# Kernel optimization log

Measured on AMD Instinct MI355X. Metric: run time of the kernel, lower is better.

## Reference

```python
import jax, jax.numpy as jnp
import numpy as np

NUM_CLASSES = 2
CONF_THRESH = 0.05
NMS_THRESH = 0.3
NMS_TOP_K = 5000
TOP_K = 750
VAR0, VAR1 = 0.1, 0.2
NEG = -1e9  # sentinel for suppressed / below-threshold scores

NUM = 16
PRIORS = 131072


def setup_inputs() -> dict:
    key = jax.random.key(0)
    k1, k2, k3 = jax.random.split(key, 3)
    loc_data = jax.random.normal(k1, (NUM, PRIORS, 4), dtype=jnp.float32)
    conf_data = jax.random.uniform(k2, (NUM * PRIORS, NUM_CLASSES), dtype=jnp.float32)
    prior_data = jax.random.uniform(k3, (PRIORS, 4), dtype=jnp.float32)
    return {"loc_data": loc_data, "conf_data": conf_data, "prior_data": prior_data}


def decode(loc, priors):
    # loc, priors: [N, 4] (cx, cy, w, h priors); SSD box decode -> (x1, y1, x2, y2)
    xy = priors[:, :2] + loc[:, :2] * VAR0 * priors[:, 2:]
    wh = priors[:, 2:] * jnp.exp(loc[:, 2:] * VAR1)
    return jnp.concatenate([xy - wh * 0.5, xy + wh * 0.5], axis=-1)


def _area(b):
    return (b[..., 2] - b[..., 0]) * (b[..., 3] - b[..., 1])


def iou_one_to_many(box, boxes):
    # box: [4], boxes: [K, 4]
    lt = jnp.maximum(box[:2], boxes[:, :2])
    rb = jnp.minimum(box[2:], boxes[:, 2:])
    wh = jnp.clip(rb - lt, 0.0)
    inter = wh[:, 0] * wh[:, 1]
    union = _area(box) + _area(boxes) - inter
    return inter / jnp.maximum(union, 1e-12)


def nms_single(boxes, scores):
    # boxes: [P, 4], scores: [P] (one image, one class) -> [TOP_K, 5] (score, x1, y1, x2, y2)
    s = jnp.where(scores > CONF_THRESH, scores, NEG)
    top_s, top_i = jax.lax.top_k(s, NMS_TOP_K)
    top_b = boxes[top_i]  # [K, 4]
    idx_range = jnp.arange(NMS_TOP_K)

    def step(s_work, _):
        idx = jnp.argmax(s_work)
        sc = s_work[idx]
        valid = sc > NEG * 0.5
        box = top_b[idx]
        ious = iou_one_to_many(box, top_b)
        kill = (ious > NMS_THRESH) | (idx_range == idx)
        s_new = jnp.where(kill, NEG, s_work)
        row = jnp.where(valid, jnp.concatenate([sc[None], box]), jnp.zeros((5,), boxes.dtype))
        return s_new, row

    _, rows = jax.lax.scan(step, top_s, None, length=TOP_K)
    return rows  # [TOP_K, 5]


def reference(loc_data, conf_data, prior_data):
    num, P, _ = loc_data.shape
    conf = conf_data.reshape(num, P, NUM_CLASSES).transpose(0, 2, 1)  # [num, C, P]
    batch_priors = jnp.broadcast_to(prior_data, (num, P, 4)).reshape(-1, 4)
    boxes = decode(loc_data.reshape(-1, 4), batch_priors).reshape(num, P, 4)
    # NMS over non-background classes, vmapped over batch and class
    per_image = jax.vmap(nms_single, in_axes=(None, 0))          # over classes
    det = jax.vmap(per_image)(boxes, conf[:, 1:, :])             # [num, C-1, TOP_K, 5]
    bg = jnp.zeros((num, 1, TOP_K, 5), det.dtype)
    return jnp.concatenate([bg, det], axis=1)                     # [num, C, TOP_K, 5]
```

## Files before the change

kernel.cpp:

```cpp
#include <hip/hip_runtime.h>
#include <cmath>

#pragma clang fp contract(off)

typedef unsigned long long ull;
typedef unsigned int uint;

#define NPRIORS 131072
#define NIMG 16
#define KSEL 5000
#define TOPK 750
#define SORTN 8192
#define MW 80
#define NCHUNK 79
#define KSELP (NCHUNK * 64)
#define NBIN 65536

#define MID03 0.30000002682209014892578125

#define WS_PAIRS 0
#define WS_NDIAG 0
#define WS_MCNT 1048576
#define WS_BOXES 1048832
#define WS_SCORES 2328832
#define WS_MASK 2649088
#define WS_HIST (WS_MASK)
#define WS_CNT  (WS_MASK + 4194304)
#define WS_POS  (WS_MASK + 8388608)
#define WS_DIAG (WS_MASK + (size_t)NIMG * KSEL * MW * 8)

__device__ inline ull readlane64(ull t, int l) {
  unsigned lo = (unsigned)__builtin_amdgcn_readlane((int)(unsigned)t, l);
  unsigned hi = (unsigned)__builtin_amdgcn_readlane((int)(unsigned)(t >> 32), l);
  return ((ull)hi << 32) | lo;
}

__device__ inline void softBarrier() {
  asm volatile("s_waitcnt lgkmcnt(0)\n\ts_barrier" ::: "memory");
}

__global__ __launch_bounds__(256) void hist_kernel(const float* __restrict__ conf,
                                                   unsigned int* __restrict__ hist) {
  const int img = blockIdx.y;
  const float4* c4 = (const float4*)conf + (size_t)img * (NPRIORS / 2);
  unsigned int* H = hist + (size_t)img * NBIN;
  for (int q = blockIdx.x * 256 + threadIdx.x; q < NPRIORS / 2; q += 64 * 256) {
    float4 v = c4[q];
    if (v.y > 0.05f) atomicAdd(&H[(__float_as_uint(v.y) >> 12) & 0xFFFFu], 1u);
    if (v.w > 0.05f) atomicAdd(&H[(__float_as_uint(v.w) >> 12) & 0xFFFFu], 1u);
  }
}

__global__ __launch_bounds__(1024) void cutoff_kernel(const unsigned int* __restrict__ hist,
                                                      unsigned int* __restrict__ pos,
                                                      int* __restrict__ meta,
                                                      float4* __restrict__ sboxes,
                                                      float* __restrict__ sscores) {
  const int img = blockIdx.x;
  const int tid = threadIdx.x;
  const int lane = tid & 63;
  const int wv = tid >> 6;
  const unsigned int* H = hist + (size_t)img * NBIN;
  unsigned int* P = pos + (size_t)img * NBIN;
  __shared__ unsigned int csum[1024];
  __shared__ unsigned int suf[1024];
  __shared__ int s_cc;
  __shared__ unsigned int s_cut, s_mc;

  for (int g = 0; g < 64; ++g) {
    unsigned int v = H[g * 1024 + tid];
    for (int m = 1; m < 64; m <<= 1) v += __shfl_xor(v, m);
    if (lane == 0) csum[g * 16 + wv] = v;
  }
  __syncthreads();
  suf[tid] = csum[tid];
  if (tid == 0) s_cc = 0;
  __syncthreads();
  for (int off = 1; off < 1024; off <<= 1) {
    unsigned int v = (tid + off < 1024) ? suf[tid + off] : 0u;
    __syncthreads();
    suf[tid] += v;
    __syncthreads();
  }
  if (suf[tid] >= KSEL && (suf[tid] - csum[tid]) < KSEL) s_cc = tid;
  __syncthreads();
  const int cc = s_cc;
  if (tid == 0) { s_cut = (unsigned int)(cc * 64); s_mc = suf[0]; }
  __syncthreads();
  for (int b = cc * 64 + tid; b < NBIN; b += 1024) {
    int q = b >> 6;
    unsigned int acc = (q + 1 < 1024) ? suf[q + 1] : 0u;
    for (int b2 = b + 1; b2 < (q + 1) * 64; ++b2) acc += H[b2];
    P[b] = acc;
    unsigned int h = H[b];
    if (acc < KSEL && acc + h >= KSEL) { s_cut = (unsigned int)b; s_mc = acc + h; }
  }
  __syncthreads();
  if (tid == 0) {
    meta[img] = (int)min(s_mc, (unsigned int)SORTN);
    meta[16 + img] = (int)s_cut;
  }
  for (int i = tid; i < KSEL; i += 1024) {
    sboxes[(size_t)img * KSEL + i] = make_float4(0.f, 0.f, 0.f, 0.f);
    sscores[(size_t)img * KSEL + i] = -1e9f;
  }
}

__global__ __launch_bounds__(256) void scatter_kernel(const float* __restrict__ conf,
                                                      const unsigned int* __restrict__ pos,
                                                      unsigned int* __restrict__ cnt,
                                                      const int* __restrict__ meta,
                                                      ull* __restrict__ pairs) {
  const int img = blockIdx.y;
  const float4* c4 = (const float4*)conf + (size_t)img * (NPRIORS / 2);
  const unsigned int* P = pos + (size_t)img * NBIN;
  unsigned int* Cn = cnt + (size_t)img * NBIN;
  ull* mypairs = pairs + (size_t)img * SORTN;
  const unsigned int cutval = ((unsigned int)meta[16 + img]) << 12;
  for (int q = blockIdx.x * 256 + threadIdx.x; q < NPRIORS / 2; q += 64 * 256) {
    float4 v = c4[q];
#pragma unroll
    for (int h = 0; h < 2; ++h) {
      float sc = h ? v.w : v.y;
      unsigned int p = 2 * (unsigned int)q + h;
      if (sc > 0.05f) {
        unsigned int u = __float_as_uint(sc);
        if (u >= cutval) {
          unsigned int bin = (u >> 12) & 0xFFFFu;
          unsigned int slot = atomicAdd(&Cn[bin], 1u);
          unsigned int idx = P[bin] + slot;
          if (idx < SORTN)
            mypairs[idx] = ((ull)u << 32) | (ull)(0xFFFFFFFFu - p);
        }
      }
    }
  }
}

__global__ __launch_bounds__(256) void rank_decode_kernel(const ull* __restrict__ pairs,
                                                          const unsigned int* __restrict__ hist,
                                                          const unsigned int* __restrict__ pos,
                                                          const int* __restrict__ meta,
                                                          const float* __restrict__ loc,
                                                          const float* __restrict__ prior,
                                                          float4* __restrict__ sboxes,
                                                          float* __restrict__ sscores) {
#pragma clang fp contract(off)
  const int img = blockIdx.y;
  const int s = blockIdx.x * 256 + threadIdx.x;
  const int mc = meta[img];
  if (s >= mc) return;
  const ull* mypairs = pairs + (size_t)img * SORTN;
  const ull key = mypairs[s];
  const unsigned int u = (unsigned int)(key >> 32);
  const unsigned int bin = (u >> 12) & 0xFFFFu;
  const unsigned int base = pos[(size_t)img * NBIN + bin];
  const unsigned int cb = hist[(size_t)img * NBIN + bin];
  const int end = min((int)(base + cb), mc);
  int rank = 0;
  for (int j = (int)base; j < end; ++j) rank += (mypairs[j] > key);
  const int fp = (int)base + rank;
  if (fp >= KSEL) return;
  const unsigned int p = 0xFFFFFFFFu - (unsigned int)(key & 0xFFFFFFFFu);
  const float* lp = loc + ((size_t)img * NPRIORS + p) * 4;
  const float* pp = prior + (size_t)p * 4;
  float l0 = lp[0], l1 = lp[1], l2 = lp[2], l3 = lp[3];
  float px = pp[0], py = pp[1], pw = pp[2], ph = pp[3];
  float cx = px + (l0 * 0.1f) * pw;
  float cy = py + (l1 * 0.1f) * ph;
  float w = pw * (float)exp((double)(l2 * 0.2f));
  float hh = ph * (float)exp((double)(l3 * 0.2f));
  float4 box;
  box.x = cx - w * 0.5f;
  box.y = cy - hh * 0.5f;
  box.z = cx + w * 0.5f;
  box.w = cy + hh * 0.5f;
  sboxes[(size_t)img * KSEL + fp] = box;
  sscores[(size_t)img * KSEL + fp] = __uint_as_float(u);
}

__global__ __launch_bounds__(256) void mask_build_kernel(const float4* __restrict__ sboxes,
                                                         ull* __restrict__ mask,
                                                         ull* __restrict__ diag,
                                                         ull* __restrict__ ndiag) {
#pragma clang fp contract(off)
  const int jt = blockIdx.x;
  const int rt = blockIdx.y;
  const int img = blockIdx.z;
  if (jt < rt) return;
  const int tid = threadIdx.x;
  const int lane = tid & 63;
  const int wv = __builtin_amdgcn_readfirstlane(tid >> 6);
  const float4* bb = sboxes + (size_t)img * KSEL;

  __shared__ float4 cbox[256];
  __shared__ float carea[256];
  {
    int j = jt * 256 + tid;
    float4 c = (j < KSEL) ? bb[j] : make_float4(0.f, 0.f, 0.f, 0.f);
    cbox[tid] = c;
    carea[tid] = (c.z - c.x) * (c.w - c.y);
  }
  __syncthreads();

  const int R = rt * 256 + wv * 64;
  if (R >= KSEL) return;
  const int i = R + lane;
  float4 pb = (i < KSEL) ? bb[i] : make_float4(0.f, 0.f, 0.f, 0.f);
  const float pa = (pb.z - pb.x) * (pb.w - pb.y);

  auto killbit = [&](int j) -> uint {
    float4 c = cbox[j];
    float caa = carea[j];
    float ltx = fmaxf(pb.x, c.x), lty = fmaxf(pb.y, c.y);
    float rbx = fminf(pb.z, c.z), rby = fminf(pb.w, c.w);
    float ww = fmaxf(rbx - ltx, 0.0f), hh = fmaxf(rby - lty, 0.0f);
    float inter = ww * hh;
    float uni = fmaxf(pa + caa - inter, 1e-12f);
    float f = fmaf(-0.3f, uni, inter);
    float band = uni * 0x1p-20f;
    bool kill = f > band;
    if (__builtin_expect(__ballot(fabsf(f) <= band) != 0ULL, 0)) {
      if (fabsf(f) <= band) kill = (double)inter > MID03 * (double)uni;
    }
    return kill ? 1u : 0u;
  };

  uint wl[4], wh[4];
#pragma unroll
  for (int s = 0; s < 4; ++s) {
    if (jt == rt && s < wv) { wl[s] = 0u; wh[s] = 0u; continue; }
    uint alo = 0, ahi = 0;
#pragma unroll 8
    for (int b = 0; b < 32; ++b) alo |= killbit(s * 64 + b) << b;
#pragma unroll 8
    for (int b = 0; b < 32; ++b) ahi |= killbit(s * 64 + 32 + b) << b;
    wl[s] = alo; wh[s] = ahi;
  }

  if (jt == rt) {
    uint mlo, mhi;
    if (lane < 32) { mlo = 0xFFFFFFFEu << lane; mhi = 0xFFFFFFFFu; }
    else           { mlo = 0u; mhi = 0xFFFFFFFEu << (lane - 32); }
    uint dl, dh;
    if (wv == 0)      { wl[0] &= mlo; wh[0] &= mhi; dl = wl[0]; dh = wh[0]; }
    else if (wv == 1) { wl[1] &= mlo; wh[1] &= mhi; dl = wl[1]; dh = wh[1]; }
    else if (wv == 2) { wl[2] &= mlo; wh[2] &= mhi; dl = wl[2]; dh = wh[2]; }
    else              { wl[3] &= mlo; wh[3] &= mhi; dl = wl[3]; dh = wh[3]; }
    if (i < KSEL) {
      diag[(size_t)img * KSELP + i] = ((ull)dh << 32) | dl;
      if (wv < 3) {
        uint nl, nh;
        if (wv == 0)      { nl = wl[1]; nh = wh[1]; }
        else if (wv == 1) { nl = wl[2]; nh = wh[2]; }
        else              { nl = wl[3]; nh = wh[3]; }
        ndiag[(size_t)img * KSELP + i] = ((ull)nh << 32) | nl;
      }
    }
  }
  if (jt == rt + 1 && wv == 3 && i < KSEL)
    ndiag[(size_t)img * KSELP + i] = ((ull)wh[0] << 32) | wl[0];

  if (i < KSEL) {
    uint* wp = (uint*)(mask + (size_t)img * KSEL * MW + (size_t)i * MW) + jt * 8;
    *(uint4*)wp = make_uint4(wl[0], wh[0], wl[1], wh[1]);
    *((uint4*)wp + 1) = make_uint4(wl[2], wh[2], wl[3], wh[3]);
  }
}

__global__ __launch_bounds__(128) void sweep_kernel(const ull* __restrict__ mask,
                                                    const ull* __restrict__ diag,
                                                    const ull* __restrict__ ndiag,
                                                    const float4* __restrict__ sboxes,
                                                    const float* __restrict__ sscores,
                                                    const int* __restrict__ meta,
                                                    float* __restrict__ out) {
  const int img = blockIdx.x;
  const int tid = threadIdx.x;
  const int lane = tid & 63;
  const bool waveA = (tid < 64);
  const int V = min(meta[img], KSEL);
  const ull* mb = mask + (size_t)img * KSEL * MW;
  const ull* dg = diag + (size_t)img * KSELP;
  const ull* ng = ndiag + (size_t)img * KSELP;
  __shared__ ull mailbox[NCHUNK + 1];
  __shared__ int pickbuf[TOPK];
  __shared__ int s_np[NCHUNK];
  __shared__ int s_start[NCHUNK];
  __shared__ int s_done;
  __shared__ int s_n;
  const int lc = min(lane, 39);

  for (int i = tid; i <= NCHUNK; i += 128) mailbox[i] = 0ULL;
  if (tid == 0) { s_done = 0; s_n = 0; }
  __syncthreads();

  if (V > 0) {
    ull dw = 0, ndw = 0, bridge = 0;
    ull rlo = 0, rhi = 0;
    int nkeep = 0;
    bool adone = false;
    if (waveA) { dw = dg[lane]; ndw = ng[lane]; }

    for (int k = 0; k < NCHUNK; ++k) {
      softBarrier();
      if (s_done) break;
      if (waveA) {
        if (!adone) {
          const int base = k * 64;
          const int nidx = min(base + 64 + lane, KSELP - 1);
          ull dwn = dg[nidx];
          ull ndwn = ng[nidx];
          ull cur = mailbox[k] | bridge;
          bridge = 0ULL;
          const int lim = V - base;
          ull validm = (lim >= 64) ? ~0ULL : ((~0ULL) >> (64 - lim));
          ull avail = (~cur) & validm;
          const int st = nkeep;
          if (lane == 0) s_start[k] = st;
          while (avail != 0ULL && nkeep < TOPK) {
            int r = __builtin_ctzll(avail);
            if (lane == 0) pickbuf[nkeep] = base + r;
            nkeep++;
            ull dr = readlane64(dw, r);
            bridge |= readlane64(ndw, r);
            avail &= ~(dr | (1ULL << r));
          }
          if (lane == 0) s_np[k] = nkeep - st;
          if (nkeep >= TOPK || base + 64 >= V) {
            if (lane == 0) { s_done = 1; s_n = (nkeep < TOPK) ? nkeep : TOPK; }
            adone = true;
          }
          dw = dwn;
          ndw = ndwn;
        }
      } else if (k >= 1) {
        const int np = s_np[k - 1];
        const int st = s_start[k - 1];
        for (int g = 0; g < np; g += 16) {
          ulonglong2 v[16];
#pragma unroll
          for (int q = 0; q < 16; ++q) {
            int t = min(g + q, np - 1);
            int row = pickbuf[st + t];
            v[q] = *(const ulonglong2*)(mb + (size_t)row * MW + 2 * lc);
          }
#pragma unroll
          for (int q = 0; q < 16; ++q) { rlo |= v[q].x; rhi |= v[q].y; }
        }
        const int w = k + 1;
        if (w < NCHUNK) {
          ull t = (w & 1) ? rhi : rlo;
          ull word = readlane64(t, w >> 1);
          if (lane == 0) mailbox[w] = word;
        }
      }
    }
  }

  __syncthreads();
  const int n = s_n;
  float* ob = out + (size_t)img * (2 * TOPK * 5) + TOPK * 5;
  for (int j = tid; j < n; j += 128) {
    int i = pickbuf[j];
    float4 b = sboxes[(size_t)img * KSEL + i];
    float sc = sscores[(size_t)img * KSEL + i];
    float* o = ob + (size_t)j * 5;
    o[0] = sc; o[1] = b.x; o[2] = b.y; o[3] = b.z; o[4] = b.w;
  }
}

extern "C" void kernel_launch(void* const* d_in, const int* in_sizes, int n_in,
                              void* d_out, int out_size, void* d_ws, size_t ws_size,
                              hipStream_t stream) {
  const float* loc = (const float*)d_in[0];
  const float* conf = (const float*)d_in[1];
  const float* prior = (const float*)d_in[2];
  float* out = (float*)d_out;

  char* ws = (char*)d_ws;
  ull* pairs = (ull*)(ws + WS_PAIRS);
  ull* ndiag = (ull*)(ws + WS_NDIAG);
  int* meta = (int*)(ws + WS_MCNT);
  float4* sboxes = (float4*)(ws + WS_BOXES);
  float* sscores = (float*)(ws + WS_SCORES);
  ull* mask = (ull*)(ws + WS_MASK);
  ull* diag = (ull*)(ws + WS_DIAG);
  unsigned int* hist = (unsigned int*)(ws + WS_HIST);
  unsigned int* cnt = (unsigned int*)(ws + WS_CNT);
  unsigned int* pos = (unsigned int*)(ws + WS_POS);

  hipMemsetAsync(d_out, 0, (size_t)out_size * sizeof(float), stream);
  hipMemsetAsync(ws + WS_HIST, 0, 2u * 4194304u, stream);

  {
    dim3 g(64, NIMG);
    hist_kernel<<<g, 256, 0, stream>>>(conf, hist);
  }
  cutoff_kernel<<<NIMG, 1024, 0, stream>>>(hist, pos, meta, sboxes, sscores);
  {
    dim3 g(64, NIMG);
    scatter_kernel<<<g, 256, 0, stream>>>(conf, pos, cnt, meta, pairs);
  }
  {
    dim3 g((SORTN + 255) / 256, NIMG);
    rank_decode_kernel<<<g, 256, 0, stream>>>(pairs, hist, pos, meta, loc, prior, sboxes, sscores);
  }
  {
    dim3 g(20, 20, NIMG);
    mask_build_kernel<<<g, 256, 0, stream>>>(sboxes, mask, diag, ndiag);
  }
  sweep_kernel<<<NIMG, 128, 0, stream>>>(mask, diag, ndiag, sboxes, sscores, meta, out);
}
```

Before: 531.2 us.

## Batch IoU mask computation, prefetch sweep diagonals deeper, drop memsets into kernels

The mask-build kernel now computes kill bits eight candidates at a time. Box loads are batched and area reads are vectorised, and there is a single ambiguity ballot per 64-column block with a whole-block double-precision fallback. The sweep kernel prefetches diagonal words two chunks ahead, makes the mailbox word wave-uniform via readfirstlane, and writes pickbuf in parallel using mbcnt ranks. The output memset and half of the workspace memset are removed: the sweep kernel zeroes its own output rows, and the cutoff kernel zeroes the count bins it uses. Together these aim to cut launch overhead and the serial critical path in the greedy sweep. In exchange, cnt is now cleared only for bins at or above the cutoff.

```diff
diff --git a/kernel.cpp b/kernel.cpp
--- a/kernel.cpp
+++ b/kernel.cpp
@@ -35,6 +35,12 @@
   return ((ull)hi << 32) | lo;
 }
 
+__device__ __forceinline__ ull rfl64(ull t) {
+  unsigned lo = (unsigned)__builtin_amdgcn_readfirstlane((int)(unsigned)t);
+  unsigned hi = (unsigned)__builtin_amdgcn_readfirstlane((int)(unsigned)(t >> 32));
+  return ((ull)hi << 32) | lo;
+}
+
 __device__ inline void softBarrier() {
   asm volatile("s_waitcnt lgkmcnt(0)\n\ts_barrier" ::: "memory");
 }
@@ -53,6 +59,7 @@
 
 __global__ __launch_bounds__(1024) void cutoff_kernel(const unsigned int* __restrict__ hist,
                                                       unsigned int* __restrict__ pos,
+                                                      unsigned int* __restrict__ cnt,
                                                       int* __restrict__ meta,
                                                       float4* __restrict__ sboxes,
                                                       float* __restrict__ sscores) {
@@ -62,6 +69,7 @@
   const int wv = tid >> 6;
   const unsigned int* H = hist + (size_t)img * NBIN;
   unsigned int* P = pos + (size_t)img * NBIN;
+  unsigned int* Cn = cnt + (size_t)img * NBIN;
   __shared__ unsigned int csum[1024];
   __shared__ unsigned int suf[1024];
   __shared__ int s_cc;
@@ -92,6 +100,7 @@
     unsigned int acc = (q + 1 < 1024) ? suf[q + 1] : 0u;
     for (int b2 = b + 1; b2 < (q + 1) * 64; ++b2) acc += H[b2];
     P[b] = acc;
+    Cn[b] = 0u;
     unsigned int h = H[b];
     if (acc < KSEL && acc + h >= KSEL) { s_cut = (unsigned int)b; s_mc = acc + h; }
   }
@@ -209,32 +218,57 @@
   float4 pb = (i < KSEL) ? bb[i] : make_float4(0.f, 0.f, 0.f, 0.f);
   const float pa = (pb.z - pb.x) * (pb.w - pb.y);
 
-  auto killbit = [&](int j) -> uint {
-    float4 c = cbox[j];
-    float caa = carea[j];
-    float ltx = fmaxf(pb.x, c.x), lty = fmaxf(pb.y, c.y);
-    float rbx = fminf(pb.z, c.z), rby = fminf(pb.w, c.w);
-    float ww = fmaxf(rbx - ltx, 0.0f), hh = fmaxf(rby - lty, 0.0f);
-    float inter = ww * hh;
-    float uni = fmaxf(pa + caa - inter, 1e-12f);
-    float f = fmaf(-0.3f, uni, inter);
-    float band = uni * 0x1p-20f;
-    bool kill = f > band;
-    if (__builtin_expect(__ballot(fabsf(f) <= band) != 0ULL, 0)) {
-      if (fabsf(f) <= band) kill = (double)inter > MID03 * (double)uni;
-    }
-    return kill ? 1u : 0u;
-  };
-
   uint wl[4], wh[4];
 #pragma unroll
   for (int s = 0; s < 4; ++s) {
     if (jt == rt && s < wv) { wl[s] = 0u; wh[s] = 0u; continue; }
     uint alo = 0, ahi = 0;
-#pragma unroll 8
-    for (int b = 0; b < 32; ++b) alo |= killbit(s * 64 + b) << b;
-#pragma unroll 8
-    for (int b = 0; b < 32; ++b) ahi |= killbit(s * 64 + 32 + b) << b;
+    ull amb = 0ULL;
+#pragma unroll
+    for (int b8 = 0; b8 < 8; ++b8) {
+      const int j0 = s * 64 + b8 * 8;
+      float4 c[8];
+      float a[8];
+#pragma unroll
+      for (int u = 0; u < 8; ++u) c[u] = cbox[j0 + u];
+      {
+        float4 a03 = *(const float4*)&carea[j0];
+        float4 a47 = *(const float4*)&carea[j0 + 4];
+        a[0] = a03.x; a[1] = a03.y; a[2] = a03.z; a[3] = a03.w;
+        a[4] = a47.x; a[5] = a47.y; a[6] = a47.z; a[7] = a47.w;
+      }
+      uint bacc = 0;
+#pragma unroll
+      for (int u = 0; u < 8; ++u) {
+        float ltx = fmaxf(pb.x, c[u].x), lty = fmaxf(pb.y, c[u].y);
+        float rbx = fminf(pb.z, c[u].z), rby = fminf(pb.w, c[u].w);
+        float ww = fmaxf(rbx - ltx, 0.0f), hh = fmaxf(rby - lty, 0.0f);
+        float inter = ww * hh;
+        float uni = fmaxf(pa + a[u] - inter, 1e-12f);
+        float f = fmaf(-0.3f, uni, inter);
+        float band = uni * 0x1p-20f;
+        bacc |= (f > band) ? (1u << u) : 0u;
+        amb |= __ballot(fabsf(f) <= band);
+      }
+      if (b8 < 4) alo |= bacc << (b8 * 8);
+      else        ahi |= bacc << (b8 * 8 - 32);
+    }
+    if (__builtin_expect(amb != 0ULL, 0)) {
+      asm volatile("" ::: "memory");
+      alo = 0; ahi = 0;
+      for (int b = 0; b < 64; ++b) {
+        float4 c = cbox[s * 64 + b];
+        float aa = carea[s * 64 + b];
+        float ltx = fmaxf(pb.x, c.x), lty = fmaxf(pb.y, c.y);
+        float rbx = fminf(pb.z, c.z), rby = fminf(pb.w, c.w);
+        float ww = fmaxf(rbx - ltx, 0.0f), hh = fmaxf(rby - lty, 0.0f);
+        float inter = ww * hh;
+        float uni = fmaxf(pa + aa - inter, 1e-12f);
+        bool kill = (double)inter > MID03 * (double)uni;
+        if (b < 32) alo |= (kill ? 1u : 0u) << b;
+        else        ahi |= (kill ? 1u : 0u) << (b - 32);
+      }
+    }
     wl[s] = alo; wh[s] = ahi;
   }
 
@@ -296,11 +330,15 @@
   __syncthreads();
 
   if (V > 0) {
-    ull dw = 0, ndw = 0, bridge = 0;
+    ull dw = 0, ndw = 0, dw1 = 0, ndw1 = 0, bridge = 0;
     ull rlo = 0, rhi = 0;
     int nkeep = 0;
     bool adone = false;
-    if (waveA) { dw = dg[lane]; ndw = ng[lane]; }
+    if (waveA) {
+      dw = dg[lane]; ndw = ng[lane];
+      const int i1 = min(64 + lane, KSELP - 1);
+      dw1 = dg[i1]; ndw1 = ng[i1];
+    }
 
     for (int k = 0; k < NCHUNK; ++k) {
       softBarrier();
@@ -308,31 +346,37 @@
       if (waveA) {
         if (!adone) {
           const int base = k * 64;
-          const int nidx = min(base + 64 + lane, KSELP - 1);
-          ull dwn = dg[nidx];
-          ull ndwn = ng[nidx];
-          ull cur = mailbox[k] | bridge;
+          const int nidx = min(base + 128 + lane, KSELP - 1);
+          ull dw2 = dg[nidx];
+          ull ndw2 = ng[nidx];
+          ull cur = rfl64(mailbox[k] | bridge);
           bridge = 0ULL;
           const int lim = V - base;
           ull validm = (lim >= 64) ? ~0ULL : ((~0ULL) >> (64 - lim));
           ull avail = (~cur) & validm;
+          ull picked = 0ULL;
           const int st = nkeep;
-          if (lane == 0) s_start[k] = st;
           while (avail != 0ULL && nkeep < TOPK) {
             int r = __builtin_ctzll(avail);
-            if (lane == 0) pickbuf[nkeep] = base + r;
+            picked |= (1ULL << r);
             nkeep++;
             ull dr = readlane64(dw, r);
             bridge |= readlane64(ndw, r);
             avail &= ~(dr | (1ULL << r));
           }
-          if (lane == 0) s_np[k] = nkeep - st;
+          {
+            uint plo = (uint)picked, phi = (uint)(picked >> 32);
+            int rank = (int)__builtin_amdgcn_mbcnt_hi(
+                phi, __builtin_amdgcn_mbcnt_lo(plo, 0u));
+            if ((picked >> lane) & 1ULL) pickbuf[st + rank] = base + lane;
+          }
+          if (lane == 0) { s_np[k] = nkeep - st; s_start[k] = st; }
           if (nkeep >= TOPK || base + 64 >= V) {
             if (lane == 0) { s_done = 1; s_n = (nkeep < TOPK) ? nkeep : TOPK; }
             adone = true;
           }
-          dw = dwn;
-          ndw = ndwn;
+          dw = dw1; ndw = ndw1;
+          dw1 = dw2; ndw1 = ndw2;
         }
       } else if (k >= 1) {
         const int np = s_np[k - 1];
@@ -360,7 +404,10 @@
 
   __syncthreads();
   const int n = s_n;
-  float* ob = out + (size_t)img * (2 * TOPK * 5) + TOPK * 5;
+  float* obase = out + (size_t)img * (2 * TOPK * 5);
+  for (int j = tid; j < TOPK * 5; j += 128) obase[j] = 0.f;
+  for (int j = TOPK * 5 + n * 5 + tid; j < 2 * TOPK * 5; j += 128) obase[j] = 0.f;
+  float* ob = obase + TOPK * 5;
   for (int j = tid; j < n; j += 128) {
     int i = pickbuf[j];
     float4 b = sboxes[(size_t)img * KSEL + i];
@@ -390,14 +437,13 @@
   unsigned int* cnt = (unsigned int*)(ws + WS_CNT);
   unsigned int* pos = (unsigned int*)(ws + WS_POS);
 
-  hipMemsetAsync(d_out, 0, (size_t)out_size * sizeof(float), stream);
-  hipMemsetAsync(ws + WS_HIST, 0, 2u * 4194304u, stream);
+  hipMemsetAsync(ws + WS_HIST, 0, 4194304u, stream);
 
   {
     dim3 g(64, NIMG);
     hist_kernel<<<g, 256, 0, stream>>>(conf, hist);
   }
-  cutoff_kernel<<<NIMG, 1024, 0, stream>>>(hist, pos, meta, sboxes, sscores);
+  cutoff_kernel<<<NIMG, 1024, 0, stream>>>(hist, pos, cnt, meta, sboxes, sscores);
   {
     dim3 g(64, NIMG);
     scatter_kernel<<<g, 256, 0, stream>>>(conf, pos, cnt, meta, pairs);
```

Result: no change. 523.2 us (-1.5%).
